# Kernel tuning notes

Measured on AMD Instinct MI355X. Metric: run time of the kernel, lower is better.

The kernel has to match this reference:

```python
import jax, jax.numpy as jnp
import numpy as np


def ste_sign(x):
    # larq ste_sign forward: sign(x) with sign(0) = 1
    return jnp.where(x >= 0, 1.0, -1.0).astype(x.dtype)


def setup_inputs() -> dict:
    key = jax.random.key(0)
    ks = jax.random.split(key, 8)
    B, H, W, Cin, Cout = 32, 56, 56, 256, 256
    x = jax.random.normal(ks[0], (B, H, W, Cin), dtype=jnp.float32)
    bias1 = jax.random.normal(ks[1], (1, 1, 1, Cin), dtype=jnp.float32) * 0.01
    kernel = jax.random.normal(ks[2], (3, 3, Cin, Cout), dtype=jnp.float32) * 0.1
    # BatchNormalization(scale=False): beta learnable, gamma=1, moving stats
    bn_beta = jax.random.normal(ks[3], (Cout,), dtype=jnp.float32) * 0.01
    bn_mean = jax.random.normal(ks[4], (Cout,), dtype=jnp.float32) * 0.01
    bn_var = jax.random.uniform(ks[5], (Cout,), dtype=jnp.float32, minval=0.5, maxval=1.5)
    bias2 = jax.random.normal(ks[6], (1, 1, 1, Cout), dtype=jnp.float32) * 0.01
    return {"x": x, "bias1": bias1, "kernel": kernel, "bn_beta": bn_beta,
            "bn_mean": bn_mean, "bn_var": bn_var, "bias2": bias2}


def reference(x, bias1, kernel, bn_beta, bn_mean, bn_var, bias2):
    eps = 1e-3  # keras BatchNormalization default epsilon
    strides = 1
    # lb_activation_1: learnable bias + ste_sign activation
    a = ste_sign(x + bias1)
    # QuantConv2D: binarize kernel, 'same' padding conv (NHWC, HWIO)
    qk = ste_sign(kernel)
    y = jax.lax.conv_general_dilated(
        a, qk, window_strides=(strides, strides), padding='SAME',
        dimension_numbers=('NHWC', 'HWIO', 'NHWC'))
    # BatchNormalization(scale=False) inference: (y - mean)/sqrt(var+eps) + beta
    y = (y - bn_mean) * jax.lax.rsqrt(bn_var + eps) + bn_beta
    # strides == 1: no avgpool residual branch
    # lb_activation_2: learnable bias + relu
    out = jax.nn.relu(y + bias2)
    return out
```

## Files before the change

### kernel.cpp

```cpp
#include <hip/hip_runtime.h>


typedef int v4i __attribute__((ext_vector_type(4)));
typedef unsigned int u32;

#define NB   32
#define HW   56
#define HP   58
#define HP2  (HP*HP)
#define CIN  256
#define COUT 256
#define NPIX (NB*HW*HW)
#define KTOT 2304
#define BM   128
#define BN   128
#define NSTEP 18
#define NWG  ((NPIX/BM)*(COUT/BN))

#define PA_BYTES ((size_t)NB*HP*HP*CIN)
#define WT_OFF   PA_BYTES
#define WT_BYTES ((size_t)KTOT*COUT)
#define SC_OFF   (WT_OFF + WT_BYTES)
#define SH_OFF   (SC_OFF + 1024)

__device__ __forceinline__ void g2l16(const void* g, void* l) {
    __builtin_amdgcn_global_load_lds(
        (const __attribute__((address_space(1))) void*)g,
        (__attribute__((address_space(3))) void*)l, 16, 0, 0);
}

__global__ __launch_bounds__(256) void pack_a_kernel(
    const float* __restrict__ x, const float* __restrict__ b1,
    signed char* __restrict__ pa)
{
    const int lane = threadIdx.x & 63;
    const int pp = blockIdx.x * 4 + (threadIdx.x >> 6);
    const int n = pp / HP2, r = pp % HP2, ph = r / HP, pw = r % HP;
    const int ci = lane * 4;
    u32 o = 0;
    if (ph >= 1 && ph <= HW && pw >= 1 && pw <= HW) {
        const int pix = (n * HW + ph - 1) * HW + (pw - 1);
        const float4 xv = *(const float4*)(x + (size_t)pix * CIN + ci);
        const float4 bv = *(const float4*)(b1 + ci);
        o  = (u32)(unsigned char)((xv.x + bv.x >= 0.f) ? 1 : -1);
        o |= (u32)(unsigned char)((xv.y + bv.y >= 0.f) ? 1 : -1) << 8;
        o |= (u32)(unsigned char)((xv.z + bv.z >= 0.f) ? 1 : -1) << 16;
        o |= (u32)(unsigned char)((xv.w + bv.w >= 0.f) ? 1 : -1) << 24;
    }
    *(u32*)(pa + (size_t)pp * CIN + ci) = o;
}

__global__ __launch_bounds__(256) void packw_kernel(
    const float* __restrict__ k, signed char* __restrict__ wf)
{
    __shared__ signed char tile[64][256];
    const int t = threadIdx.x, k0 = blockIdx.x * 64;
    for (int j = 0; j < 64; ++j)
        tile[j][t] = (k[(size_t)(k0 + j) * COUT + t] >= 0.f) ? 1 : -1;
    __syncthreads();
    u32 wd[16];
#pragma unroll
    for (int j = 0; j < 16; ++j) wd[j] = 0;
#pragma unroll
    for (int j = 0; j < 64; ++j)
        wd[j >> 2] |= ((u32)(unsigned char)tile[j][t]) << ((j & 3) * 8);
#pragma unroll
    for (int c = 0; c < 4; ++c)
        *(uint4*)(wf + (((size_t)blockIdx.x * 4 + c) * 256 + t) * 16) =
            make_uint4(wd[4*c], wd[4*c+1], wd[4*c+2], wd[4*c+3]);
}

__global__ __launch_bounds__(256) void bnprep_kernel(
    const float* __restrict__ beta, const float* __restrict__ mean,
    const float* __restrict__ var, const float* __restrict__ b2,
    float* __restrict__ scale, float* __restrict__ shift)
{
    const int t = threadIdx.x;
    const float s = rsqrtf(var[t] + 1e-3f);
    scale[t] = s;
    shift[t] = beta[t] - mean[t] * s + b2[t];
}

__global__ __launch_bounds__(256, 2) void conv_mfma_kernel(
    const signed char* __restrict__ pa, const signed char* __restrict__ wf,
    const float* __restrict__ scale, const float* __restrict__ shift,
    float* __restrict__ out)
{
    __shared__ signed char L[2][16384];

    const int t = threadIdx.x, l = t & 63, v = t >> 6;
    const int vm = v >> 1, vn = v & 1;
    const int swz  = (blockIdx.x & 7) * (NWG / 8) + (blockIdx.x >> 3);
    const int tile = swz >> 1;
    const int co0  = (swz & 1) << 7;
    const int p0 = tile * BM;

    const signed char* abase[2];
#pragma unroll
    for (int i = 0; i < 2; ++i) {
        const int q = (t >> 2) + i * 64;
        const int p = p0 + q;
        const int n = p / 3136, r = p % 3136, h = r / 56, w = r % 56;
        const int aswz = (((t & 3) ^ ((q >> 1) & 3)) << 4);
        abase[i] = pa + ((size_t)(n * HP + h) * HP + w) * CIN + aswz;
    }

    int aoff[4];
#pragma unroll
    for (int pg = 0; pg < 4; ++pg) {
        const int row = vm * 64 + pg * 16 + (l & 15);
        aoff[pg] = row * 64 + ((((l >> 4) ^ (row >> 1)) & 3) << 4);
    }
    u32 boffg[4];
#pragma unroll
    for (int cg = 0; cg < 4; ++cg) {
        const int co = co0 + vn * 64 + cg * 16 + (l & 15);
        boffg[cg] = (u32)((((l >> 4) * 256) + co) * 16);
    }

    v4i acc[4][4];
#pragma unroll
    for (int i = 0; i < 4; ++i)
#pragma unroll
        for (int j = 0; j < 4; ++j) acc[i][j] = (v4i){0, 0, 0, 0};

    auto goffA = [&](int k64) {
        const int tap = k64 >> 2, cq = k64 & 3;
        const int ty = tap / 3, tx = tap - ty * 3;
        return ((ty * HP + tx) << 8) + (cq << 6);
    };
    auto STAGE = [&](int buf, int s) {
#pragma unroll
        for (int ks = 0; ks < 2; ++ks) {
            const int k64 = 2 * s + ks;
            const int go = goffA(k64);
            g2l16(abase[0] + go, &L[buf][ks * 8192 + v * 1024]);
            g2l16(abase[1] + go, &L[buf][ks * 8192 + 4096 + v * 1024]);
        }
    };

    STAGE(0, 0);
    asm volatile("s_waitcnt vmcnt(0)" ::: "memory");
    __builtin_amdgcn_s_barrier();

#pragma unroll 1
    for (int s = 0; s < NSTEP; ++s) {
        const int cur = s & 1, nxt = cur ^ 1;
        const signed char* Lc = &L[cur][0];
        if (s + 1 < NSTEP) STAGE(nxt, s + 1);
        v4i af[2][4], bf[2][4];
#pragma unroll
        for (int ks = 0; ks < 2; ++ks) {
            const u32 kbase = (u32)(2 * s + ks) * 16384;
#pragma unroll
            for (int cg = 0; cg < 4; ++cg)
                bf[ks][cg] = *(const v4i*)(wf + kbase + boffg[cg]);
#pragma unroll
            for (int pg = 0; pg < 4; ++pg)
                af[ks][pg] = *(const v4i*)(Lc + ks * 8192 + aoff[pg]);
        }
        __builtin_amdgcn_s_setprio(1);
#pragma unroll
        for (int ks = 0; ks < 2; ++ks)
#pragma unroll
            for (int pg = 0; pg < 4; ++pg)
#pragma unroll
                for (int cg = 0; cg < 4; ++cg)
                    acc[pg][cg] = __builtin_amdgcn_mfma_i32_16x16x64_i8(
                        af[ks][pg], bf[ks][cg], acc[pg][cg], 0, 0, 0);
        __builtin_amdgcn_s_setprio(0);
        asm volatile("s_waitcnt vmcnt(0)" ::: "memory");
        __builtin_amdgcn_s_barrier();
    }

#pragma unroll
    for (int cg = 0; cg < 4; ++cg) {
        const int co = co0 + vn * 64 + cg * 16 + (l & 15);
        const float sc = scale[co], sh = shift[co];
#pragma unroll
        for (int pg = 0; pg < 4; ++pg) {
            const int prow0 = p0 + vm * 64 + pg * 16 + (l >> 4) * 4;
#pragma unroll
            for (int rr = 0; rr < 4; ++rr) {
                const float y = (float)acc[pg][cg][rr];
                out[(size_t)(prow0 + rr) * COUT + co] = fmaxf(fmaf(y, sc, sh), 0.f);
            }
        }
    }
}

extern "C" void kernel_launch(void* const* d_in, const int* in_sizes, int n_in,
                              void* d_out, int out_size, void* d_ws, size_t ws_size,
                              hipStream_t stream)
{
    const float* x      = (const float*)d_in[0];
    const float* bias1  = (const float*)d_in[1];
    const float* kernel = (const float*)d_in[2];
    const float* bn_beta = (const float*)d_in[3];
    const float* bn_mean = (const float*)d_in[4];
    const float* bn_var  = (const float*)d_in[5];
    const float* bias2   = (const float*)d_in[6];
    float* out = (float*)d_out;

    signed char* pa  = (signed char*)d_ws;
    signed char* wfp = (signed char*)d_ws + WT_OFF;
    float* scale = (float*)((char*)d_ws + SC_OFF);
    float* shift = (float*)((char*)d_ws + SH_OFF);

    pack_a_kernel<<<dim3(NB * HP2 / 4), dim3(256), 0, stream>>>(x, bias1, pa);
    packw_kernel<<<dim3(KTOT / 64), dim3(256), 0, stream>>>(kernel, wfp);
    bnprep_kernel<<<dim3(1), dim3(256), 0, stream>>>(bn_beta, bn_mean, bn_var, bias2,
                                                     scale, shift);
    conv_mfma_kernel<<<dim3(NWG), dim3(256), 0, stream>>>(pa, wfp, scale, shift, out);
}
```

Baseline: 99.10 us.

## Give each wave a private LDS A-tile and drop block barriers

Each wave now stages its own 64 activation rows into a private 16 KB LDS region through direct global-to-LDS loads. This replaces the shared 128-row tile and removes the per-step workgroup barrier. Partial vmcnt waits now let the weight-fragment loads and the next-stage prefetch stay in flight while only the current stage's LDS data is awaited. In exchange, waves sharing the same pixel rows fetch those activations twice, which doubles A-side global/L2 traffic. LDS use per block grows to 64 KB.

```diff
diff --git a/kernel.cpp b/kernel.cpp
--- a/kernel.cpp
+++ b/kernel.cpp
@@ -86,30 +86,31 @@
     const float* __restrict__ scale, const float* __restrict__ shift,
     float* __restrict__ out)
 {
-    __shared__ signed char L[2][16384];
-
-    const int t = threadIdx.x, l = t & 63, v = t >> 6;
-    const int vm = v >> 1, vn = v & 1;
+    __shared__ signed char L[65536];
+
+    const int t = threadIdx.x, l = t & 63, w = t >> 6;
+    const int vm = w >> 1, vn = w & 1;
     const int swz  = (blockIdx.x & 7) * (NWG / 8) + (blockIdx.x >> 3);
     const int tile = swz >> 1;
     const int co0  = (swz & 1) << 7;
     const int p0 = tile * BM;
-
-    const signed char* abase[2];
-#pragma unroll
-    for (int i = 0; i < 2; ++i) {
-        const int q = (t >> 2) + i * 64;
-        const int p = p0 + q;
-        const int n = p / 3136, r = p % 3136, h = r / 56, w = r % 56;
-        const int aswz = (((t & 3) ^ ((q >> 1) & 3)) << 4);
-        abase[i] = pa + ((size_t)(n * HP + h) * HP + w) * CIN + aswz;
+    const int wb = w * 16384;
+
+    const signed char* abase[4];
+#pragma unroll
+    for (int j = 0; j < 4; ++j) {
+        const int rl = j * 16 + (l >> 2);
+        const int p  = p0 + vm * 64 + rl;
+        const int n = p / 3136, r = p % 3136, h = r / 56, ww = r % 56;
+        const int aswz = (((l & 3) ^ ((rl >> 1) & 3)) << 4);
+        abase[j] = pa + ((size_t)(n * HP + h) * HP + ww) * CIN + aswz;
     }
 
     int aoff[4];
 #pragma unroll
     for (int pg = 0; pg < 4; ++pg) {
-        const int row = vm * 64 + pg * 16 + (l & 15);
-        aoff[pg] = row * 64 + ((((l >> 4) ^ (row >> 1)) & 3) << 4);
+        const int rl = pg * 16 + (l & 15);
+        aoff[pg] = rl * 64 + ((((l >> 4) ^ (rl >> 1)) & 3) << 4);
     }
     u32 boffg[4];
 #pragma unroll
@@ -132,33 +133,40 @@
     auto STAGE = [&](int buf, int s) {
 #pragma unroll
         for (int ks = 0; ks < 2; ++ks) {
-            const int k64 = 2 * s + ks;
-            const int go = goffA(k64);
-            g2l16(abase[0] + go, &L[buf][ks * 8192 + v * 1024]);
-            g2l16(abase[1] + go, &L[buf][ks * 8192 + 4096 + v * 1024]);
+            const int go = goffA(2 * s + ks);
+#pragma unroll
+            for (int j = 0; j < 4; ++j)
+                g2l16(abase[j] + go, &L[wb + buf * 8192 + ks * 4096 + j * 1024]);
         }
     };
 
     STAGE(0, 0);
-    asm volatile("s_waitcnt vmcnt(0)" ::: "memory");
-    __builtin_amdgcn_s_barrier();
 
 #pragma unroll 1
     for (int s = 0; s < NSTEP; ++s) {
         const int cur = s & 1, nxt = cur ^ 1;
-        const signed char* Lc = &L[cur][0];
-        if (s + 1 < NSTEP) STAGE(nxt, s + 1);
-        v4i af[2][4], bf[2][4];
+        const bool pre = (s + 1 < NSTEP);
+
+        v4i bf[2][4];
 #pragma unroll
         for (int ks = 0; ks < 2; ++ks) {
-            const u32 kbase = (u32)(2 * s + ks) * 16384;
+            const u32 kb = (u32)(2 * s + ks) * 16384;
 #pragma unroll
             for (int cg = 0; cg < 4; ++cg)
-                bf[ks][cg] = *(const v4i*)(wf + kbase + boffg[cg]);
+                bf[ks][cg] = *(const v4i*)(wf + kb + boffg[cg]);
+        }
+        if (pre) STAGE(nxt, s + 1);
+
+        if (pre) { asm volatile("s_waitcnt vmcnt(16)" ::: "memory"); }
+        else     { asm volatile("s_waitcnt vmcnt(8)"  ::: "memory"); }
+
+        v4i af[2][4];
+#pragma unroll
+        for (int ks = 0; ks < 2; ++ks)
 #pragma unroll
             for (int pg = 0; pg < 4; ++pg)
-                af[ks][pg] = *(const v4i*)(Lc + ks * 8192 + aoff[pg]);
-        }
+                af[ks][pg] = *(const v4i*)(&L[wb + cur * 8192 + ks * 4096 + aoff[pg]]);
+
         __builtin_amdgcn_s_setprio(1);
 #pragma unroll
         for (int ks = 0; ks < 2; ++ks)
@@ -169,8 +177,6 @@
                     acc[pg][cg] = __builtin_amdgcn_mfma_i32_16x16x64_i8(
                         af[ks][pg], bf[ks][cg], acc[pg][cg], 0, 0, 0);
         __builtin_amdgcn_s_setprio(0);
-        asm volatile("s_waitcnt vmcnt(0)" ::: "memory");
-        __builtin_amdgcn_s_barrier();
     }
 
 #pragma unroll
```

Result: slower. 109.8 us (+10.8%).

## Load A fragments directly from global memory, dropping LDS staging and barriers

Applied to the files above, without the earlier changes.

Removes the LDS double-buffered staging of the packed activation tile. Each wave now reads its A fragments straight from global memory (through the cache), just as it already does for the weights. This drops the per-step barriers and vmcnt waits, and with no shared memory in use the launch-bounds occupancy hint goes from 2 to 3. The cost is that waves sharing the same pixels read them redundantly from global/L2, and there is no explicit prefetch, so global load latency sits right in front of the MFMAs each step.

```diff
diff --git a/kernel.cpp b/kernel.cpp
--- a/kernel.cpp
+++ b/kernel.cpp
@@ -22,12 +22,6 @@
 #define WT_BYTES ((size_t)KTOT*COUT)
 #define SC_OFF   (WT_OFF + WT_BYTES)
 #define SH_OFF   (SC_OFF + 1024)
-
-__device__ __forceinline__ void g2l16(const void* g, void* l) {
-    __builtin_amdgcn_global_load_lds(
-        (const __attribute__((address_space(1))) void*)g,
-        (__attribute__((address_space(3))) void*)l, 16, 0, 0);
-}
 
 __global__ __launch_bounds__(256) void pack_a_kernel(
     const float* __restrict__ x, const float* __restrict__ b1,
@@ -81,13 +75,11 @@
     shift[t] = beta[t] - mean[t] * s + b2[t];
 }
 
-__global__ __launch_bounds__(256, 2) void conv_mfma_kernel(
+__global__ __launch_bounds__(256, 3) void conv_mfma_kernel(
     const signed char* __restrict__ pa, const signed char* __restrict__ wf,
     const float* __restrict__ scale, const float* __restrict__ shift,
     float* __restrict__ out)
 {
-    __shared__ signed char L[2][16384];
-
     const int t = threadIdx.x, l = t & 63, v = t >> 6;
     const int vm = v >> 1, vn = v & 1;
     const int swz  = (blockIdx.x & 7) * (NWG / 8) + (blockIdx.x >> 3);
@@ -95,21 +87,12 @@
     const int co0  = (swz & 1) << 7;
     const int p0 = tile * BM;
 
-    const signed char* abase[2];
-#pragma unroll
-    for (int i = 0; i < 2; ++i) {
-        const int q = (t >> 2) + i * 64;
-        const int p = p0 + q;
-        const int n = p / 3136, r = p % 3136, h = r / 56, w = r % 56;
-        const int aswz = (((t & 3) ^ ((q >> 1) & 3)) << 4);
-        abase[i] = pa + ((size_t)(n * HP + h) * HP + w) * CIN + aswz;
-    }
-
-    int aoff[4];
+    u32 aB[4];
 #pragma unroll
     for (int pg = 0; pg < 4; ++pg) {
-        const int row = vm * 64 + pg * 16 + (l & 15);
-        aoff[pg] = row * 64 + ((((l >> 4) ^ (row >> 1)) & 3) << 4);
+        const int p = p0 + vm * 64 + pg * 16 + (l & 15);
+        const int n = p / 3136, r = p % 3136, h = r / 56, w = r % 56;
+        aB[pg] = (u32)((((n * HP + h) * HP + w) << 8) + ((l >> 4) << 4));
     }
     u32 boffg[4];
 #pragma unroll
@@ -127,38 +110,28 @@
     auto goffA = [&](int k64) {
         const int tap = k64 >> 2, cq = k64 & 3;
         const int ty = tap / 3, tx = tap - ty * 3;
-        return ((ty * HP + tx) << 8) + (cq << 6);
+        return (u32)(((ty * HP + tx) << 8) + (cq << 6));
     };
-    auto STAGE = [&](int buf, int s) {
-#pragma unroll
-        for (int ks = 0; ks < 2; ++ks) {
-            const int k64 = 2 * s + ks;
-            const int go = goffA(k64);
-            g2l16(abase[0] + go, &L[buf][ks * 8192 + v * 1024]);
-            g2l16(abase[1] + go, &L[buf][ks * 8192 + 4096 + v * 1024]);
-        }
-    };
-
-    STAGE(0, 0);
-    asm volatile("s_waitcnt vmcnt(0)" ::: "memory");
-    __builtin_amdgcn_s_barrier();
 
 #pragma unroll 1
     for (int s = 0; s < NSTEP; ++s) {
-        const int cur = s & 1, nxt = cur ^ 1;
-        const signed char* Lc = &L[cur][0];
-        if (s + 1 < NSTEP) STAGE(nxt, s + 1);
+        const u32 go0 = goffA(2 * s);
+        const u32 go1 = goffA(2 * s + 1);
+        const u32 kb0 = (u32)(2 * s) * 16384;
+        const u32 kb1 = kb0 + 16384;
+
         v4i af[2][4], bf[2][4];
 #pragma unroll
-        for (int ks = 0; ks < 2; ++ks) {
-            const u32 kbase = (u32)(2 * s + ks) * 16384;
+        for (int pg = 0; pg < 4; ++pg) {
+            af[0][pg] = *(const v4i*)(pa + aB[pg] + go0);
+            af[1][pg] = *(const v4i*)(pa + aB[pg] + go1);
+        }
 #pragma unroll
-            for (int cg = 0; cg < 4; ++cg)
-                bf[ks][cg] = *(const v4i*)(wf + kbase + boffg[cg]);
-#pragma unroll
-            for (int pg = 0; pg < 4; ++pg)
-                af[ks][pg] = *(const v4i*)(Lc + ks * 8192 + aoff[pg]);
+        for (int cg = 0; cg < 4; ++cg) {
+            bf[0][cg] = *(const v4i*)(wf + kb0 + boffg[cg]);
+            bf[1][cg] = *(const v4i*)(wf + kb1 + boffg[cg]);
         }
+
         __builtin_amdgcn_s_setprio(1);
 #pragma unroll
         for (int ks = 0; ks < 2; ++ks)
@@ -169,8 +142,6 @@
                     acc[pg][cg] = __builtin_amdgcn_mfma_i32_16x16x64_i8(
                         af[ks][pg], bf[ks][cg], acc[pg][cg], 0, 0, 0);
         __builtin_amdgcn_s_setprio(0);
-        asm volatile("s_waitcnt vmcnt(0)" ::: "memory");
-        __builtin_amdgcn_s_barrier();
     }
 
 #pragma unroll
```

New measurement: 173.7 us. 75.3% more time.
